# Optimization experiments

Measured on AMD Instinct MI355X. Metric: run time of the kernel, lower is better.

## Reference

```python
import jax, jax.numpy as jnp
import numpy as np

# dims
T, INPUT_DIM = 128, 512
C_INT, ISQ, DIM, C = 8, 16, 256, 8  # internal_channels, input_square_dim, dim, n_channel
OSQ, OUT_CH = 8, 16                  # output_square_dim, output_size // osq^2
INPUT_SCALE, S1, S2 = 1.0, 0.9, 0.1
K1, D1, K2, D2 = 3, 1, 5, 2


def dw_circ_conv(x, w, dilation):
    """Depthwise conv with circular padding. x: [B,C,H,W], w: [C,1,k,k]."""
    k = w.shape[-1]
    pad = dilation * (k - 1) // 2
    xp = jnp.pad(x, ((0, 0), (0, 0), (pad, pad), (pad, pad)), mode='wrap')
    return jax.lax.conv_general_dilated(
        xp, w, window_strides=(1, 1), padding='VALID',
        rhs_dilation=(dilation, dilation), feature_group_count=x.shape[1])


def setup_inputs() -> dict:
    key = jax.random.key(0)
    ks = jax.random.split(key, 10)
    X = jax.random.normal(ks[0], (T, INPUT_DIM), jnp.float32)
    # nn.Linear weight [out, in]
    W_embed = jax.random.normal(ks[1], (C_INT * ISQ * ISQ, INPUT_DIM), jnp.float32) * 0.02
    mask_coarse = jax.random.bernoulli(ks[2], 0.5, (1, 1, ISQ, ISQ)).astype(jnp.float32)
    mask_fine = jax.random.bernoulli(ks[3], 0.5, (1, 1, DIM, DIM)).astype(jnp.float32)
    # ConvTranspose2d weight [in_ch, out_ch, k, k], k = dim // isq = 16
    W_deconv = jax.random.normal(ks[4], (C_INT, C, DIM // ISQ, DIM // ISQ), jnp.float32) * 0.02

    def lateral_w(k, ksz, p):
        # LateralConnections with conn_exp=1: |w| * bernoulli(p), normalized per output channel
        w = jnp.abs(jax.random.normal(k, (C, 1, ksz, ksz), jnp.float32))
        m = jax.random.bernoulli(jax.random.fold_in(k, 1), p, w.shape).astype(jnp.float32)
        w = w * m
        return w / w.sum(axis=(1, 2, 3), keepdims=True)

    w1 = lateral_w(ks[5], K1, 0.9)
    w2 = lateral_w(ks[6], K2, 0.9)
    # output Conv2d: [out_ch, in_ch, k, k], k = dim // osq = 32
    w_out = jax.random.normal(ks[7], (OUT_CH, C, DIM // OSQ, DIM // OSQ), jnp.float32) * 0.01
    b_out = jax.random.normal(ks[8], (OUT_CH,), jnp.float32) * 0.01
    return dict(X=X, W_embed=W_embed, mask_coarse=mask_coarse, mask_fine=mask_fine,
                W_deconv=W_deconv, w1=w1, w2=w2, w_out=w_out, b_out=b_out)


def reference(X, W_embed, mask_coarse, mask_fine, W_deconv, w1, w2, w_out, b_out):
    t = X.shape[0]
    ksz = W_deconv.shape[-1]
    # CorticalInput
    u = (X @ W_embed.T).reshape(t, C_INT, ISQ, ISQ) * mask_coarse  # [T,Cint,isq,isq]
    # ConvTranspose2d with stride == kernel_size (non-overlapping) == block expansion
    u = jnp.einsum('tcij,coab->toiajb', u, W_deconv).reshape(t, C, ISQ * ksz, ISQ * ksz)
    u = INPUT_SCALE * u * mask_fine  # [T,C,dim,dim]

    # sequential reservoir scan
    def step(Z, x):
        Z = jnp.tanh(S1 * dw_circ_conv(Z, w1, D1) + S2 * dw_circ_conv(Z, w2, D2) + x)
        return Z, Z[0]

    Z0 = jnp.zeros((1, C, DIM, DIM), X.dtype)
    _, outs = jax.lax.scan(step, Z0, u)  # outs: [T,C,dim,dim]

    # readout conv (kernel == stride == dim // osq)
    ko = w_out.shape[-1]
    y = jax.lax.conv_general_dilated(outs, w_out, (ko, ko), 'VALID')
    y = y + b_out[None, :, None, None]
    return y.reshape(t, -1)
```

## Files before the change

### kernel.cpp

```cpp
#include <hip/hip_runtime.h>
#include <math.h>

#define SB_OFF   0
#define E_OFF    524288

typedef float vf4 __attribute__((ext_vector_type(4)));

__device__ __forceinline__ float fast_tanh(float x) {
  x = fminf(fmaxf(x, -15.f), 15.f);
  float ex = __expf(2.f * x);
  return __fdividef(ex - 1.f, ex + 1.f);
}

template <int CTRL>
__device__ __forceinline__ float dpp_add(float v) {
  int x = __builtin_amdgcn_update_dpp(0, __float_as_int(v), CTRL, 0xF, 0xF, true);
  return v + __int_as_float(x);
}

__device__ __forceinline__ void st16(float* p, float a, float b, float c, float d) {
  vf4 v; v.x = a; v.y = b; v.z = c; v.w = d;
  asm volatile("global_store_dwordx4 %0, %1, off sc0 sc1" :: "v"(p), "v"(v) : "memory");
}
__device__ __forceinline__ vf4 ld16(const float* p) {
  vf4 r;
  asm volatile("global_load_dwordx4 %0, %1, off sc0 sc1\n"
               "s_waitcnt vmcnt(0)"
               : "=&v"(r) : "v"(p) : "memory");
  return r;
}
__device__ __forceinline__ void tag_store(unsigned* p, unsigned v) {
  asm volatile("s_waitcnt vmcnt(0)\n"
               "global_store_dword %0, %1, off sc0 sc1" :: "v"(p), "v"(v) : "memory");
}

__global__ __launch_bounds__(256) void prep_kernel(
    const float* __restrict__ X, const float* __restrict__ W_embed,
    const float* __restrict__ mask_coarse, const float* __restrict__ b_out,
    float* __restrict__ ws, float* __restrict__ out)
{
  __shared__ float Xl[128][36];
  __shared__ float Wl[8][36];

  const int tid = threadIdx.x, bid = blockIdx.x;
  float* eb = ws + E_OFF;

  {
    int idx = bid * 512 + tid * 2;
    out[idx]     = b_out[(idx >> 6) & 15];
    out[idx + 1] = b_out[((idx + 1) >> 6) & 15];
  }

  const int o0 = bid * 8;
  const int ol = tid & 7;
  const int tg = tid >> 3;
  float acc[4] = {0.f, 0.f, 0.f, 0.f};

  for (int k0 = 0; k0 < 512; k0 += 32) {
    __syncthreads();
#pragma unroll
    for (int p = 0; p < 4; ++p) {
      int tr = p * 32 + (tid >> 3);
      int kc = (tid & 7) * 4;
      *(float4*)&Xl[tr][kc] = *(const float4*)&X[(size_t)tr * 512 + k0 + kc];
    }
    if (tid < 64) {
      int wr = tid >> 3, wc = (tid & 7) * 4;
      *(float4*)&Wl[wr][wc] = *(const float4*)&W_embed[(size_t)(o0 + wr) * 512 + k0 + wc];
    }
    __syncthreads();
#pragma unroll
    for (int kk = 0; kk < 8; ++kk) {
      float4 w4 = *(const float4*)&Wl[ol][kk * 4];
#pragma unroll
      for (int i = 0; i < 4; ++i) {
        float4 x4 = *(const float4*)&Xl[tg * 4 + i][kk * 4];
        acc[i] = fmaf(w4.x, x4.x, fmaf(w4.y, x4.y, fmaf(w4.z, x4.z, fmaf(w4.w, x4.w, acc[i]))));
      }
    }
  }
  const int o = o0 + ol;
  float mc = mask_coarse[o & 255];
#pragma unroll
  for (int i = 0; i < 4; ++i)
    eb[(size_t)(tg * 4 + i) * 2048 + o] = acc[i] * mc;
}

__global__ __launch_bounds__(512, 2) void scan_kernel(
    const float* __restrict__ mask_fine, const float* __restrict__ W_deconv,
    const float* __restrict__ w1, const float* __restrict__ w2,
    const float* __restrict__ w_out, float* __restrict__ ws,
    float* __restrict__ out)
{
  __shared__ float zin[2][72 * 44];
  __shared__ float rowbuf[2][64 * 17];

  const int tid  = threadIdx.x;
  const int bid  = blockIdx.x;
  const int ch   = bid >> 5;
  const int tile = bid & 31;
  const int tI = tile >> 3, tJ = tile & 7;
  const int r0 = tI << 6, c0 = tJ << 5;
  const int row = tid >> 3;
  const int cg  = tid & 7;
  const int lc  = cg << 2;

  float* Zb = ws + SB_OFF;
  const float* eb = ws + E_OFF;
  const int myoff = (ch * 32 + tile) << 10;

  const int i0 = (r0 + row) >> 4;
  const int jj = (c0 + lc) >> 4;
  float4 wd[8];
#pragma unroll
  for (int c = 0; c < 8; ++c)
    wd[c] = *(const float4*)&W_deconv[(((c * 8 + ch) * 16) + (row & 15)) * 16 + (lc & 15)];
  float4 mf = *(const float4*)&mask_fine[(size_t)(r0 + row) * 256 + c0 + lc];
  float4 wo[16];
#pragma unroll
  for (int oc = 0; oc < 16; ++oc)
    wo[oc] = *(const float4*)&w_out[(((oc * 8 + ch) * 32) + (row & 31)) * 32 + lc];
  float w1s[9], w2s[25];
#pragma unroll
  for (int k = 0; k < 9; ++k)
    w1s[k] = __uint_as_float(__builtin_amdgcn_readfirstlane(__float_as_uint(w1[ch * 9 + k])));
#pragma unroll
  for (int k = 0; k < 25; ++k)
    w2s[k] = __uint_as_float(__builtin_amdgcn_readfirstlane(__float_as_uint(w2[ch * 25 + k])));

  int rd_src = 0, rd_dst = 0, rd_tag = 0;
  const bool hasrd = (tid < 208);
  if (hasrd) {
    int u = tid, di = 0, dj = 0, src = 0, dst = 0, wv = 0;
    if (u < 32) {
      di = -1; src = 128 + (u >> 3) * 32 + (u & 7) * 4;
      dst = (u >> 3) * 44 + 4 + (u & 7) * 4; wv = 7;
    } else if (u < 64) {
      int v = u - 32; di = 1; src = (v >> 3) * 32 + (v & 7) * 4;
      dst = (68 + (v >> 3)) * 44 + 4 + (v & 7) * 4; wv = 0;
    } else if (u < 128) {
      int v = u - 64; dj = -1; src = 512 + v * 4; dst = (4 + v) * 44; wv = v >> 3;
    } else if (u < 192) {
      int v = u - 128; dj = 1; src = 256 + v * 4; dst = (4 + v) * 44 + 36; wv = v >> 3;
    } else {
      int v = u - 192, c = v >> 2, r = v & 3;
      if (c == 0)      { di = -1; dj = -1; src = 816 + r * 4; dst = r * 44;            wv = 7; }
      else if (c == 1) { di = -1; dj = 1;  src = 800 + r * 4; dst = r * 44 + 36;       wv = 7; }
      else if (c == 2) { di = 1;  dj = -1; src = 784 + r * 4; dst = (68 + r) * 44;     wv = 0; }
      else             { di = 1;  dj = 1;  src = 768 + r * 4; dst = (68 + r) * 44 + 36; wv = 0; }
    }
    int nI = (tI + di) & 3, nJ = (tJ + dj) & 7;
    int roff = (ch * 32 + nI * 8 + nJ) << 10;
    rd_src = roff + src;
    rd_tag = roff + 832 + wv * 16;
    rd_dst = dst;
  }

  for (int k = tid; k < 2 * 72 * 44; k += 512) zin[0][k] = 0.f;
  __syncthreads();

  for (int t = 0; t < 128; ++t) {
    float* sb = Zb + (size_t)((t + 1) & 1) * 262144;
    const float* zr = zin[t & 1];
    float*       zw = zin[(t + 1) & 1];
    float*       rb = rowbuf[t & 1];

    float ev[8];
#pragma unroll
    for (int c = 0; c < 8; ++c)
      ev[c] = eb[(size_t)t * 2048 + c * 256 + i0 * 16 + jj];

    float c1a[4] = {0, 0, 0, 0}, c2a[4] = {0, 0, 0, 0};
    {
      float w[12];
      auto load_row = [&](int zrr) {
        float4 A  = *(const float4*)&zr[zrr * 44 + lc];
        float4 B  = *(const float4*)&zr[zrr * 44 + lc + 4];
        float4 Cq = *(const float4*)&zr[zrr * 44 + lc + 8];
        w[0]=A.x; w[1]=A.y; w[2]=A.z; w[3]=A.w;
        w[4]=B.x; w[5]=B.y; w[6]=B.z; w[7]=B.w;
        w[8]=Cq.x; w[9]=Cq.y; w[10]=Cq.z; w[11]=Cq.w;
      };
      auto k2row = [&](int a) {
#pragma unroll
        for (int j = 0; j < 4; ++j)
#pragma unroll
          for (int b = 0; b < 5; ++b)
            c2a[j] = fmaf(w[j + 2 * b], w2s[a * 5 + b], c2a[j]);
      };
      auto k1row = [&](int a) {
#pragma unroll
        for (int j = 0; j < 4; ++j)
#pragma unroll
          for (int b = 0; b < 3; ++b)
            c1a[j] = fmaf(w[j + 3 + b], w1s[a * 3 + b], c1a[j]);
      };
      load_row(row + 0); k2row(0);
      load_row(row + 2); k2row(1);
      load_row(row + 3); k1row(0);
      load_row(row + 4); k1row(1); k2row(2);
      load_row(row + 5); k1row(2);
      load_row(row + 6); k2row(3);
      load_row(row + 8); k2row(4);
    }
    float zv[4];
    {
      const float* mfp = (const float*)&mf;
#pragma unroll
      for (int j = 0; j < 4; ++j) {
        float u = 0.f;
#pragma unroll
        for (int c = 0; c < 8; ++c)
          u = fmaf(ev[c], ((const float*)&wd[c])[j], u);
        float val = fmaf(0.9f, c1a[j], fmaf(0.1f, c2a[j], mfp[j] * u));
        zv[j] = fast_tanh(val);
      }
    }

    if (t < 127) {
      float* rec = sb + myoff;
      if (row < 4)   st16(rec + row * 32 + lc, zv[0], zv[1], zv[2], zv[3]);
      if (row >= 60) st16(rec + 128 + (row - 60) * 32 + lc, zv[0], zv[1], zv[2], zv[3]);
      if (lc == 0)   st16(rec + 256 + row * 4, zv[0], zv[1], zv[2], zv[3]);
      if (lc == 28)  st16(rec + 512 + row * 4, zv[0], zv[1], zv[2], zv[3]);
      if (row < 4 && lc == 0)   st16(rec + 768 + row * 4, zv[0], zv[1], zv[2], zv[3]);
      if (row < 4 && lc == 28)  st16(rec + 784 + row * 4, zv[0], zv[1], zv[2], zv[3]);
      if (row >= 60 && lc == 0) st16(rec + 800 + (row - 60) * 4, zv[0], zv[1], zv[2], zv[3]);
      if (row >= 60 && lc == 28) st16(rec + 816 + (row - 60) * 4, zv[0], zv[1], zv[2], zv[3]);
      if ((tid & 63) == 0)
        tag_store((unsigned*)(rec + 832 + (tid >> 6) * 16), (unsigned)(t + 1));
    }

    *(float4*)&zw[(4 + row) * 44 + 4 + lc] = make_float4(zv[0], zv[1], zv[2], zv[3]);

    float racc[16];
#pragma unroll
    for (int oc = 0; oc < 16; ++oc) {
      const float* wop = (const float*)&wo[oc];
      racc[oc] = fmaf(zv[0], wop[0], fmaf(zv[1], wop[1], fmaf(zv[2], wop[2], zv[3] * wop[3])));
    }
#pragma unroll
    for (int k = 0; k < 16; ++k) {
      racc[k] = dpp_add<0xB1>(racc[k]);
      racc[k] = dpp_add<0x4E>(racc[k]);
      racc[k] = dpp_add<0x141>(racc[k]);
    }
    rb[row * 17 + (cg << 1)]     = racc[cg << 1];
    rb[row * 17 + (cg << 1) + 1] = racc[(cg << 1) + 1];

    if (t < 127 && hasrd) {
      const unsigned tg = (unsigned)(t + 1);
      const unsigned* ta = (const unsigned*)(sb + rd_tag);
      int spins = 0;
      while (__hip_atomic_load(ta, __ATOMIC_RELAXED, __HIP_MEMORY_SCOPE_AGENT) != tg) {
        __builtin_amdgcn_s_sleep(1);
        if (++spins > (1 << 18)) break;
      }
      vf4 v = ld16(sb + rd_src);
      zw[rd_dst]     = v.x;
      zw[rd_dst + 1] = v.y;
      zw[rd_dst + 2] = v.z;
      zw[rd_dst + 3] = v.w;
    }

    __syncthreads();

    if (tid < 32) {
      int p = tid >> 4, oc = tid & 15;
      float s = 0.f;
#pragma unroll
      for (int r = 0; r < 32; ++r) s += rb[(p * 32 + r) * 17 + oc];
      atomicAdd(&out[t * 1024 + oc * 64 + (2 * tI + p) * 8 + tJ], s);
    }
  }
}

extern "C" void kernel_launch(void* const* d_in, const int* in_sizes, int n_in,
                              void* d_out, int out_size, void* d_ws, size_t ws_size,
                              hipStream_t stream) {
  const float* X           = (const float*)d_in[0];
  const float* W_embed     = (const float*)d_in[1];
  const float* mask_coarse = (const float*)d_in[2];
  const float* mask_fine   = (const float*)d_in[3];
  const float* W_deconv    = (const float*)d_in[4];
  const float* w1          = (const float*)d_in[5];
  const float* w2          = (const float*)d_in[6];
  const float* w_out       = (const float*)d_in[7];
  const float* b_out       = (const float*)d_in[8];
  float* ws  = (float*)d_ws;
  float* out = (float*)d_out;

  prep_kernel<<<dim3(256), dim3(256), 0, stream>>>(X, W_embed, mask_coarse, b_out, ws, out);
  scan_kernel<<<dim3(256), dim3(512), 0, stream>>>(mask_fine, W_deconv, w1, w2, w_out, ws, out);
}
```

Measured before the change: 508.5 us.

## Replace tag-then-data halo exchange with self-tagged data+flag packets

Each halo value is now stored together with its step tag as a 64-bit packet, so consumers poll the data directly instead of waiting on a separate tag and then reloading. This removes the store-side vmcnt wait before the tag store and the extra dependent load round trip on the reader side. In exchange, halo traffic doubles in size, there are more store instructions per producing thread, twice as many reader threads take part, and the prep kernel must zero the tag slots.

```diff
diff --git a/kernel.cpp b/kernel.cpp
--- a/kernel.cpp
+++ b/kernel.cpp
@@ -2,9 +2,12 @@
 #include <math.h>
 
 #define SB_OFF   0
-#define E_OFF    524288
+#define REC      1664
+#define PAR      425984
+#define E_OFF    851968
 
 typedef float vf4 __attribute__((ext_vector_type(4)));
+typedef float vf2 __attribute__((ext_vector_type(2)));
 
 __device__ __forceinline__ float fast_tanh(float x) {
   x = fminf(fmaxf(x, -15.f), 15.f);
@@ -18,20 +21,22 @@
   return v + __int_as_float(x);
 }
 
-__device__ __forceinline__ void st16(float* p, float a, float b, float c, float d) {
-  vf4 v; v.x = a; v.y = b; v.z = c; v.w = d;
-  asm volatile("global_store_dwordx4 %0, %1, off sc0 sc1" :: "v"(p), "v"(v) : "memory");
-}
-__device__ __forceinline__ vf4 ld16(const float* p) {
-  vf4 r;
-  asm volatile("global_load_dwordx4 %0, %1, off sc0 sc1\n"
-               "s_waitcnt vmcnt(0)"
-               : "=&v"(r) : "v"(p) : "memory");
-  return r;
-}
-__device__ __forceinline__ void tag_store(unsigned* p, unsigned v) {
-  asm volatile("s_waitcnt vmcnt(0)\n"
-               "global_store_dword %0, %1, off sc0 sc1" :: "v"(p), "v"(v) : "memory");
+__device__ __forceinline__ void st_pkt(float* p, float d, unsigned tag) {
+  vf2 v; v.x = d; v.y = __uint_as_float(tag);
+  asm volatile("global_store_dwordx2 %0, %1, off sc0 sc1" :: "v"(p), "v"(v) : "memory");
+}
+__device__ __forceinline__ void poll2(const float* p, unsigned want, float* d0, float* d1) {
+  vf2 a, b; int spins = 0;
+  for (;;) {
+    asm volatile("global_load_dwordx2 %0, %2, off sc0 sc1\n"
+                 "global_load_dwordx2 %1, %2, off offset:8 sc0 sc1\n"
+                 "s_waitcnt vmcnt(0)"
+                 : "=&v"(a), "=&v"(b) : "v"(p) : "memory");
+    if (__float_as_uint(a.y) == want && __float_as_uint(b.y) == want) break;
+    __builtin_amdgcn_s_sleep(1);
+    if (++spins > (1 << 18)) break;
+  }
+  *d0 = a.x; *d1 = b.x;
 }
 
 __global__ __launch_bounds__(256) void prep_kernel(
@@ -44,6 +49,11 @@
 
   const int tid = threadIdx.x, bid = blockIdx.x;
   float* eb = ws + E_OFF;
+
+  for (int f = tid; f < 832; f += 256) {
+    ws[SB_OFF + (size_t)bid * REC + 2 * f + 1]       = 0.f;
+    ws[SB_OFF + PAR + (size_t)bid * REC + 2 * f + 1] = 0.f;
+  }
 
   {
     int idx = bid * 512 + tid * 2;
@@ -107,7 +117,7 @@
 
   float* Zb = ws + SB_OFF;
   const float* eb = ws + E_OFF;
-  const int myoff = (ch * 32 + tile) << 10;
+  const int myoff = bid * REC;
 
   const int i0 = (r0 + row) >> 4;
   const int jj = (c0 + lc) >> 4;
@@ -128,31 +138,36 @@
   for (int k = 0; k < 25; ++k)
     w2s[k] = __uint_as_float(__builtin_amdgcn_readfirstlane(__float_as_uint(w2[ch * 25 + k])));
 
-  int rd_src = 0, rd_dst = 0, rd_tag = 0;
-  const bool hasrd = (tid < 208);
+  int rd_src = 0, rd_dst = 0;
+  const bool hasrd = (tid < 416);
   if (hasrd) {
-    int u = tid, di = 0, dj = 0, src = 0, dst = 0, wv = 0;
-    if (u < 32) {
-      di = -1; src = 128 + (u >> 3) * 32 + (u & 7) * 4;
-      dst = (u >> 3) * 44 + 4 + (u & 7) * 4; wv = 7;
-    } else if (u < 64) {
-      int v = u - 32; di = 1; src = (v >> 3) * 32 + (v & 7) * 4;
-      dst = (68 + (v >> 3)) * 44 + 4 + (v & 7) * 4; wv = 0;
+    int u = tid, di = 0, dj = 0, chunk = 0, dst = 0;
+    if (u < 64) {
+      di = -1; chunk = 64 + u;
+      int r = u >> 4, c = (u * 2) & 31;
+      dst = r * 44 + 4 + c;
     } else if (u < 128) {
-      int v = u - 64; dj = -1; src = 512 + v * 4; dst = (4 + v) * 44; wv = v >> 3;
-    } else if (u < 192) {
-      int v = u - 128; dj = 1; src = 256 + v * 4; dst = (4 + v) * 44 + 36; wv = v >> 3;
+      int v = u - 64; di = 1; chunk = v;
+      int r = v >> 4, c = (v * 2) & 31;
+      dst = (68 + r) * 44 + 4 + c;
+    } else if (u < 256) {
+      int v = u - 128; dj = -1; chunk = 256 + v;
+      int r = v >> 1, c = (v & 1) * 2;
+      dst = (4 + r) * 44 + c;
+    } else if (u < 384) {
+      int v = u - 256; dj = 1; chunk = 128 + v;
+      int r = v >> 1, c = (v & 1) * 2;
+      dst = (4 + r) * 44 + 36 + c;
     } else {
-      int v = u - 192, c = v >> 2, r = v & 3;
-      if (c == 0)      { di = -1; dj = -1; src = 816 + r * 4; dst = r * 44;            wv = 7; }
-      else if (c == 1) { di = -1; dj = 1;  src = 800 + r * 4; dst = r * 44 + 36;       wv = 7; }
-      else if (c == 2) { di = 1;  dj = -1; src = 784 + r * 4; dst = (68 + r) * 44;     wv = 0; }
-      else             { di = 1;  dj = 1;  src = 768 + r * 4; dst = (68 + r) * 44 + 36; wv = 0; }
+      int v = u - 384, cc = v >> 3, k = v & 7;
+      int r = k >> 1, c2 = (k & 1) * 2;
+      if (cc == 0)      { di = -1; dj = -1; chunk = 408 + k; dst = r * 44 + c2; }
+      else if (cc == 1) { di = -1; dj = 1;  chunk = 400 + k; dst = r * 44 + 36 + c2; }
+      else if (cc == 2) { di = 1;  dj = -1; chunk = 392 + k; dst = (68 + r) * 44 + c2; }
+      else              { di = 1;  dj = 1;  chunk = 384 + k; dst = (68 + r) * 44 + 36 + c2; }
     }
     int nI = (tI + di) & 3, nJ = (tJ + dj) & 7;
-    int roff = (ch * 32 + nI * 8 + nJ) << 10;
-    rd_src = roff + src;
-    rd_tag = roff + 832 + wv * 16;
+    rd_src = (ch * 32 + nI * 8 + nJ) * REC + chunk * 4;
     rd_dst = dst;
   }
 
@@ -160,7 +175,7 @@
   __syncthreads();
 
   for (int t = 0; t < 128; ++t) {
-    float* sb = Zb + (size_t)((t + 1) & 1) * 262144;
+    float* sb = Zb + (size_t)((t + 1) & 1) * PAR;
     const float* zr = zin[t & 1];
     float*       zw = zin[(t + 1) & 1];
     float*       rb = rowbuf[t & 1];
@@ -219,16 +234,47 @@
 
     if (t < 127) {
       float* rec = sb + myoff;
-      if (row < 4)   st16(rec + row * 32 + lc, zv[0], zv[1], zv[2], zv[3]);
-      if (row >= 60) st16(rec + 128 + (row - 60) * 32 + lc, zv[0], zv[1], zv[2], zv[3]);
-      if (lc == 0)   st16(rec + 256 + row * 4, zv[0], zv[1], zv[2], zv[3]);
-      if (lc == 28)  st16(rec + 512 + row * 4, zv[0], zv[1], zv[2], zv[3]);
-      if (row < 4 && lc == 0)   st16(rec + 768 + row * 4, zv[0], zv[1], zv[2], zv[3]);
-      if (row < 4 && lc == 28)  st16(rec + 784 + row * 4, zv[0], zv[1], zv[2], zv[3]);
-      if (row >= 60 && lc == 0) st16(rec + 800 + (row - 60) * 4, zv[0], zv[1], zv[2], zv[3]);
-      if (row >= 60 && lc == 28) st16(rec + 816 + (row - 60) * 4, zv[0], zv[1], zv[2], zv[3]);
-      if ((tid & 63) == 0)
-        tag_store((unsigned*)(rec + 832 + (tid >> 6) * 16), (unsigned)(t + 1));
+      const unsigned tg = (unsigned)(t + 1);
+      if (row < 4) {
+        float* p = rec + 2 * (row * 32 + lc);
+#pragma unroll
+        for (int j = 0; j < 4; ++j) st_pkt(p + 2 * j, zv[j], tg);
+      }
+      if (row >= 60) {
+        float* p = rec + 2 * (128 + (row - 60) * 32 + lc);
+#pragma unroll
+        for (int j = 0; j < 4; ++j) st_pkt(p + 2 * j, zv[j], tg);
+      }
+      if (lc == 0) {
+        float* p = rec + 2 * (256 + row * 4);
+#pragma unroll
+        for (int j = 0; j < 4; ++j) st_pkt(p + 2 * j, zv[j], tg);
+      }
+      if (lc == 28) {
+        float* p = rec + 2 * (512 + row * 4);
+#pragma unroll
+        for (int j = 0; j < 4; ++j) st_pkt(p + 2 * j, zv[j], tg);
+      }
+      if (row < 4 && lc == 0) {
+        float* p = rec + 2 * (768 + row * 4);
+#pragma unroll
+        for (int j = 0; j < 4; ++j) st_pkt(p + 2 * j, zv[j], tg);
+      }
+      if (row < 4 && lc == 28) {
+        float* p = rec + 2 * (784 + row * 4);
+#pragma unroll
+        for (int j = 0; j < 4; ++j) st_pkt(p + 2 * j, zv[j], tg);
+      }
+      if (row >= 60 && lc == 0) {
+        float* p = rec + 2 * (800 + (row - 60) * 4);
+#pragma unroll
+        for (int j = 0; j < 4; ++j) st_pkt(p + 2 * j, zv[j], tg);
+      }
+      if (row >= 60 && lc == 28) {
+        float* p = rec + 2 * (816 + (row - 60) * 4);
+#pragma unroll
+        for (int j = 0; j < 4; ++j) st_pkt(p + 2 * j, zv[j], tg);
+      }
     }
 
     *(float4*)&zw[(4 + row) * 44 + 4 + lc] = make_float4(zv[0], zv[1], zv[2], zv[3]);
@@ -249,18 +295,10 @@
     rb[row * 17 + (cg << 1) + 1] = racc[(cg << 1) + 1];
 
     if (t < 127 && hasrd) {
-      const unsigned tg = (unsigned)(t + 1);
-      const unsigned* ta = (const unsigned*)(sb + rd_tag);
-      int spins = 0;
-      while (__hip_atomic_load(ta, __ATOMIC_RELAXED, __HIP_MEMORY_SCOPE_AGENT) != tg) {
-        __builtin_amdgcn_s_sleep(1);
-        if (++spins > (1 << 18)) break;
-      }
-      vf4 v = ld16(sb + rd_src);
-      zw[rd_dst]     = v.x;
-      zw[rd_dst + 1] = v.y;
-      zw[rd_dst + 2] = v.z;
-      zw[rd_dst + 3] = v.w;
+      float d0, d1;
+      poll2(sb + rd_src, (unsigned)(t + 1), &d0, &d1);
+      zw[rd_dst]     = d0;
+      zw[rd_dst + 1] = d1;
     }
 
     __syncthreads();
```

New measurement: 560.1 us. 1.1x slower.
